# Kernel optimization log

Measured on AMD Instinct MI355X. Metric: run time of the kernel, lower is better.

Reference implementation:

```python
import jax, jax.numpy as jnp
import numpy as np

N = 100000   # nodes
E = 1600000  # edges
D_IN, D_H, D_OUT = 128, 128, 64
BN_EPS = 1e-5


def setup_inputs() -> dict:
    key = jax.random.key(0)
    ks = jax.random.split(key, 12)

    def lin_w(k, fan_in, shape):
        s = 1.0 / np.sqrt(fan_in)
        return jax.random.uniform(k, shape, jnp.float32, -s, s)

    return {
        "x": jax.random.normal(ks[0], (N, D_IN), jnp.float32),
        "edge_index": jax.random.randint(ks[1], (2, E), 0, N, dtype=jnp.int64),
        "edge_weight": jax.random.uniform(ks[2], (E,), jnp.float32),
        "W1": lin_w(ks[3], D_IN, (D_IN, D_H)),
        "b1": jnp.zeros((D_H,), jnp.float32),
        "W2": lin_w(ks[4], D_H, (D_H, D_H)),
        "b2": jnp.zeros((D_H,), jnp.float32),
        "W3": lin_w(ks[5], D_H, (D_H, D_OUT)),
        "b3": jnp.zeros((D_OUT,), jnp.float32),
        "gamma1": jnp.ones((D_H,), jnp.float32),
        "beta1": jnp.zeros((D_H,), jnp.float32),
        "gamma2": jnp.ones((D_H,), jnp.float32),
        "beta2": jnp.zeros((D_H,), jnp.float32),
    }


def _gcn_conv(x, src, dst, w, W, b):
    # PyG GCNConv: x' = D^{-1/2} (A + I) D^{-1/2} (x W) + b, self-loop weight 1
    n = x.shape[0]
    h = x @ W                                   # [N, d_out]
    loop = jnp.arange(n, dtype=src.dtype)
    s = jnp.concatenate([src, loop])            # [E+N]
    d = jnp.concatenate([dst, loop])
    ww = jnp.concatenate([w, jnp.ones((n,), w.dtype)])
    deg = jax.ops.segment_sum(ww, d, num_segments=n)          # in-degree at targets
    dinv = jnp.where(deg > 0, jax.lax.rsqrt(deg), 0.0)
    norm = dinv[s] * ww * dinv[d]               # [E+N]
    msg = h[s] * norm[:, None]                  # gather + scale
    out = jax.ops.segment_sum(msg, d, num_segments=n)
    return out + b


def _batch_norm(x, gamma, beta):
    mean = jnp.mean(x, axis=0)
    var = jnp.mean(jnp.square(x - mean), axis=0)  # biased, as BatchNorm uses
    return (x - mean) * jax.lax.rsqrt(var + BN_EPS) * gamma + beta


def reference(x, edge_index, edge_weight, W1, b1, W2, b2, W3, b3,
              gamma1, beta1, gamma2, beta2):
    src, dst = edge_index[0], edge_index[1]
    h = _gcn_conv(x, src, dst, edge_weight, W1, b1)
    h = jax.nn.relu(_batch_norm(h, gamma1, beta1))
    h = _gcn_conv(h, src, dst, edge_weight, W2, b2)
    h = jax.nn.relu(_batch_norm(h, gamma2, beta2))
    return _gcn_conv(h, src, dst, edge_weight, W3, b3)
```

## Files before the change

### kernel.cpp

```cpp
#include <hip/hip_runtime.h>
#include <hip/hip_fp16.h>
#include <cstdint>
#include <cstddef>

#define BN_EPS 1e-5f
#define KB 256
#define BSH 9

typedef _Float16 half8 __attribute__((ext_vector_type(8)));
typedef float floatx4 __attribute__((ext_vector_type(4)));

__device__ __forceinline__ float loadS(const __half* p) { return __half2float(*p); }
__device__ __forceinline__ float2 load2(const __half* p) {
    return __half22float2(*(const __half2*)p);
}
__device__ __forceinline__ void storeS(float* p, float v) { *p = v; }
__device__ __forceinline__ void storeS(__half* p, float v) { *p = __float2half(v); }
__device__ __forceinline__ void store2(float* p, float a, float b) {
    *(float2*)p = make_float2(a, b);
}
__device__ __forceinline__ void store2(__half* p, float a, float b) {
    *(__half2*)p = __floats2half2_rn(a, b);
}
__device__ __forceinline__ float wn_of(unsigned v) {
    __half_raw hr; hr.x = (unsigned short)(v & 0x7fffu);
    return __half2float((__half)hr);
}

static __device__ __forceinline__ int load_edge(const void* ei, int mode64, long long pos) {
    if (mode64) return (int)((const long long*)ei)[pos];
    return ((const int*)ei)[pos];
}

__global__ __launch_bounds__(256) void init_kernel(const unsigned* __restrict__ eiw, int nwords,
                                                   int* __restrict__ mode,
                                                   unsigned* __restrict__ pc,
                                                   const float* __restrict__ W1,
                                                   const float* __restrict__ W2,
                                                   const float* __restrict__ W3,
                                                   _Float16* __restrict__ WT1,
                                                   _Float16* __restrict__ WT2,
                                                   _Float16* __restrict__ WT3) {
    __shared__ unsigned red[256];
    const int bid = (int)blockIdx.x;
    const int tid = (int)threadIdx.x;
    if (bid < 64) {
        uint4 z = make_uint4(0, 0, 0, 0);
        *(uint4*)&pc[bid * 1024 + tid * 4] = z;
        return;
    }
    if (bid == 64) {
        unsigned m = 0;
        for (int i = 1 + 2 * tid; i < nwords; i += 512) m |= eiw[i];
        red[tid] = m;
        __syncthreads();
        for (int s = 128; s > 0; s >>= 1) {
            if (tid < s) red[tid] |= red[tid + s];
            __syncthreads();
        }
        if (tid == 0) mode[0] = (red[0] == 0) ? 1 : 0;
        return;
    }
    const int t_ = bid - 65;
    if (t_ < 64) {
        int t = t_ * 256 + tid;
        int n = t / 128, k = t % 128;
        WT1[t] = (_Float16)W1[k * 128 + n];
    } else if (t_ < 128) {
        int t = (t_ - 64) * 256 + tid;
        int n = t / 128, k = t % 128;
        WT2[t] = (_Float16)W2[k * 128 + n];
    } else {
        int t = (t_ - 128) * 256 + tid;
        int n = t / 128, k = t % 128;
        WT3[t] = (_Float16)W3[k * 64 + n];
    }
}

__global__ __launch_bounds__(256) void coarse_hist_kernel(const void* __restrict__ ei,
                                                          const int* __restrict__ mode,
                                                          unsigned* __restrict__ pc,
                                                          int E, int epb) {
    __shared__ unsigned h[256];
    const int k = (int)blockIdx.x;
    const int tid = (int)threadIdx.x;
    h[tid] = 0;
    __syncthreads();
    const int md = *mode;
    const int e0 = k * epb;
    const int e1 = min(E, e0 + epb);
    for (int e = e0 + tid; e < e1; e += 256) {
        int d = load_edge(ei, md, (long long)E + e);
        atomicAdd(&h[d >> BSH], 1u);
    }
    __syncthreads();
    pc[k * 256 + tid] = h[tid];
}

__global__ __launch_bounds__(256) void scan_pc_kernel(unsigned* __restrict__ pc,
                                                      int* __restrict__ tb) {
    __shared__ int red[256];
    const int b = (int)blockIdx.x;
    const int tid = (int)threadIdx.x;
    const unsigned v = pc[tid * 256 + b];
    red[tid] = (int)v;
    __syncthreads();
    for (int off = 1; off < 256; off <<= 1) {
        int t = 0;
        if (tid >= off) t = red[tid - off];
        __syncthreads();
        red[tid] += t;
        __syncthreads();
    }
    pc[tid * 256 + b] = (unsigned)(red[tid] - (int)v);
    if (tid == 255) tb[b] = red[255];
}

__global__ __launch_bounds__(256) void scan_buckets_kernel(const int* __restrict__ tb,
                                                           int* __restrict__ bbase, int nbuck,
                                                           float* __restrict__ gsum,
                                                           float* __restrict__ gsq) {
    __shared__ int red[256];
    const int tid = (int)threadIdx.x;
    const int v = (tid < nbuck) ? tb[tid] : 0;
    red[tid] = v;
    __syncthreads();
    for (int off = 1; off < 256; off <<= 1) {
        int t = 0;
        if (tid >= off) t = red[tid - off];
        __syncthreads();
        red[tid] += t;
        __syncthreads();
    }
    bbase[tid] = red[tid] - v;
    if (tid < 128) { gsum[tid] = 0.0f; gsq[tid] = 0.0f; }
}

template <int M, bool BN, typename TI>
__device__ __forceinline__ void gemm_body(int gbid, const TI* __restrict__ X,
                                          const _Float16* __restrict__ WTg,
                                          const float* __restrict__ sc,
                                          const float* __restrict__ sh,
                                          __half* __restrict__ Hout, int N,
                                          _Float16* WT ) {
    constexpr int CT = M / 16;
    constexpr int LDK = 136;

    for (int t = threadIdx.x; t < M * 16; t += 256) {
        int n = t / 16, seg = t % 16;
        *(half8*)&WT[n * LDK + seg * 8] = *(const half8*)&WTg[n * 128 + seg * 8];
    }
    __syncthreads();

    const int wave = (int)threadIdx.x >> 6;
    const int lane = (int)threadIdx.x & 63;
    const int qd = lane >> 4;
    const int ln = lane & 15;
    const int tile0 = gbid * 64 + wave * 16;
    int ar = tile0 + ln;
    if (ar >= N) ar = N - 1;

    half8 aF[4];
    const TI* xr = X + (size_t)ar * 128 + qd * 8;
#pragma unroll
    for (int kb = 0; kb < 4; ++kb) {
        float vv[8];
        if constexpr (sizeof(TI) == 4) {
            float4 v0 = *(const float4*)(xr + kb * 32);
            float4 v1 = *(const float4*)(xr + kb * 32 + 4);
            vv[0] = v0.x; vv[1] = v0.y; vv[2] = v0.z; vv[3] = v0.w;
            vv[4] = v1.x; vv[5] = v1.y; vv[6] = v1.z; vv[7] = v1.w;
        } else {
            half8 raw = *(const half8*)(xr + kb * 32);
#pragma unroll
            for (int j = 0; j < 8; ++j) vv[j] = (float)raw[j];
        }
        if (BN) {
            const int kbase = kb * 32 + qd * 8;
#pragma unroll
            for (int j = 0; j < 8; ++j)
                vv[j] = fmaxf(fmaf(vv[j], sc[kbase + j], sh[kbase + j]), 0.0f);
        }
        half8 a;
#pragma unroll
        for (int j = 0; j < 8; ++j) a[j] = (_Float16)vv[j];
        aF[kb] = a;
    }

#pragma unroll
    for (int ct = 0; ct < CT; ++ct) {
        floatx4 acc = {0.0f, 0.0f, 0.0f, 0.0f};
#pragma unroll
        for (int kb = 0; kb < 4; ++kb) {
            half8 b = *(const half8*)&WT[(ct * 16 + ln) * LDK + kb * 32 + qd * 8];
            acc = __builtin_amdgcn_mfma_f32_16x16x32_f16(aF[kb], b, acc, 0, 0, 0);
        }
#pragma unroll
        for (int r = 0; r < 4; ++r) {
            int orow = tile0 + qd * 4 + r;
            if (orow < N) Hout[(size_t)orow * M + ct * 16 + ln] = __float2half(acc[r]);
        }
    }
}

__global__ __launch_bounds__(256) void sort_gemm1_kernel(const void* __restrict__ ei,
                                                         const float* __restrict__ ew,
                                                         const unsigned* __restrict__ pc,
                                                         const int* __restrict__ bbase,
                                                         unsigned long long* __restrict__ sortedE,
                                                         const int* __restrict__ mode, int E,
                                                         int epb, int GB,
                                                         const float* __restrict__ X,
                                                         const _Float16* __restrict__ WT1g,
                                                         __half* __restrict__ Hout, int N) {
    __shared__ _Float16 WT[128 * 136];
    __shared__ unsigned off_s[256];
    if ((int)blockIdx.x < GB) {
        gemm_body<128, false, float>(blockIdx.x, X, WT1g, nullptr, nullptr, Hout, N, WT);
        return;
    }
    const int k = (int)blockIdx.x - GB;
    const int tid = (int)threadIdx.x;
    off_s[tid] = (unsigned)bbase[tid] + pc[k * 256 + tid];
    __syncthreads();
    const int md = *mode;
    const int e0 = k * epb;
    const int e1 = min(E, e0 + epb);
    for (int e = e0 + tid; e < e1; e += 256) {
        int d = load_edge(ei, md, (long long)E + e);
        int s = load_edge(ei, md, e);
        float wv = ew[e];
        unsigned slot = atomicAdd(&off_s[d >> BSH], 1u);
        sortedE[slot] = ((unsigned long long)(unsigned)d << 33) |
                        ((unsigned long long)(unsigned)s << 16) |
                        (unsigned long long)(unsigned short)__half_as_ushort(__float2half(wv));
    }
}

__global__ __launch_bounds__(256) void csr_build_kernel(const unsigned long long* __restrict__ sortedE,
                                                        const int* __restrict__ bbase,
                                                        const int* __restrict__ tb,
                                                        float* __restrict__ dinv,
                                                        int* __restrict__ cnt,
                                                        int* __restrict__ row_start,
                                                        unsigned* __restrict__ edata, int N) {
    __shared__ unsigned cs[512];
    __shared__ float ws[512];
    __shared__ float dv[512];
    __shared__ unsigned sc[512];
    __shared__ unsigned cur[512];
    __shared__ int red[256];
    const int b = (int)blockIdx.x;
    const int tid = (int)threadIdx.x;
    const int n0 = b << BSH;
    const int base = bbase[b];
    const int len = tb[b];

    cs[tid] = 0; cs[tid + 256] = 0;
    ws[tid] = 0.0f; ws[tid + 256] = 0.0f;
    cur[tid] = 0; cur[tid + 256] = 0;
    __syncthreads();

    for (int i = tid; i < len; i += 256) {
        unsigned long long p = sortedE[base + i];
        unsigned fine = (unsigned)(p >> 33) - (unsigned)n0;
        atomicAdd(&cs[fine], 1u);
        __half_raw hr; hr.x = (unsigned short)(p & 0xFFFFu);
        atomicAdd(&ws[fine], __half2float((__half)hr));
    }
    __syncthreads();

    const unsigned a0 = cs[2 * tid];
    const unsigned a1 = cs[2 * tid + 1];
    const int s2 = (int)(a0 + a1);
    red[tid] = s2;
    __syncthreads();
    for (int off = 1; off < 256; off <<= 1) {
        int t = 0;
        if (tid >= off) t = red[tid - off];
        __syncthreads();
        red[tid] += t;
        __syncthreads();
    }
    const int excl2 = red[tid] - s2;
    sc[2 * tid] = (unsigned)excl2;
    sc[2 * tid + 1] = (unsigned)(excl2 + (int)a0);

#pragma unroll
    for (int q = 0; q < 2; ++q) {
        const int f = tid + q * 256;
        const int node = n0 + f;
        const float dvv = rsqrtf(1.0f + ws[f]);
        dv[f] = dvv;
        if (node < N) {
            dinv[node] = dvv;
            cnt[node] = (int)cs[f];
            row_start[node] = base + (int)sc[f];
        }
    }
    __syncthreads();

    for (int i = tid; i < len; i += 256) {
        unsigned long long p = sortedE[base + i];
        unsigned fine = (unsigned)(p >> 33) - (unsigned)n0;
        unsigned s = (unsigned)(p >> 16) & 0x1FFFFu;
        __half_raw hr; hr.x = (unsigned short)(p & 0xFFFFu);
        float wnp = __half2float((__half)hr) * dv[fine];
        unsigned r = atomicAdd(&cur[fine], 1u);
        unsigned hb = (unsigned)__half_as_ushort(__float2half(wnp)) & 0x7fffu;
        edata[base + (int)sc[fine] + (int)r] = (s << 15) | hb;
    }
}

template <int D, bool BIAS, typename TY>
__global__ __launch_bounds__(256) void agg_kernel(const __half* __restrict__ H,
                                                  const unsigned* __restrict__ edata,
                                                  const int* __restrict__ row_start,
                                                  const int* __restrict__ cnt,
                                                  const float* __restrict__ dinv,
                                                  const float* __restrict__ bias,
                                                  TY* __restrict__ Y, int N) {
    constexpr int VPT = D / 64;
    const int lane = (int)threadIdx.x & 63;
    const int i = (int)blockIdx.x * 4 + ((int)threadIdx.x >> 6);
    if (i >= N) return;
    const int c0 = lane * VPT;
    const float di = dinv[i];
    const float dii = di * di;

    float acc0, acc1 = 0.0f;
    if constexpr (VPT == 2) {
        float2 h = load2(H + (size_t)i * D + c0);
        acc0 = dii * h.x;
        acc1 = dii * h.y;
    } else {
        acc0 = dii * loadS(H + (size_t)i * D + c0);
    }

    const int base = row_start[i];
    const int n = cnt[i];
    for (int off = 0; off < n; off += 64) {
        const int rem = n - off;
        unsigned ev = 0;
        if (lane < rem) ev = edata[base + off + lane];
        const int mm = min(64, rem);
        for (int j = 0; j < mm; j += 8) {
            const unsigned e0 = __shfl(ev, j),     e1 = __shfl(ev, j + 1);
            const unsigned e2 = __shfl(ev, j + 2), e3 = __shfl(ev, j + 3);
            const unsigned e4 = __shfl(ev, j + 4), e5 = __shfl(ev, j + 5);
            const unsigned e6 = __shfl(ev, j + 6), e7 = __shfl(ev, j + 7);
            const float w0 = dinv[e0 >> 15] * wn_of(e0);
            const float w1 = dinv[e1 >> 15] * wn_of(e1);
            const float w2 = dinv[e2 >> 15] * wn_of(e2);
            const float w3 = dinv[e3 >> 15] * wn_of(e3);
            const float w4 = dinv[e4 >> 15] * wn_of(e4);
            const float w5 = dinv[e5 >> 15] * wn_of(e5);
            const float w6 = dinv[e6 >> 15] * wn_of(e6);
            const float w7 = dinv[e7 >> 15] * wn_of(e7);
            if constexpr (VPT == 2) {
                float2 h0 = load2(H + (size_t)(e0 >> 15) * D + c0);
                float2 h1 = load2(H + (size_t)(e1 >> 15) * D + c0);
                float2 h2 = load2(H + (size_t)(e2 >> 15) * D + c0);
                float2 h3 = load2(H + (size_t)(e3 >> 15) * D + c0);
                float2 h4 = load2(H + (size_t)(e4 >> 15) * D + c0);
                float2 h5 = load2(H + (size_t)(e5 >> 15) * D + c0);
                float2 h6 = load2(H + (size_t)(e6 >> 15) * D + c0);
                float2 h7 = load2(H + (size_t)(e7 >> 15) * D + c0);
                acc0 = fmaf(w0, h0.x, acc0); acc1 = fmaf(w0, h0.y, acc1);
                acc0 = fmaf(w1, h1.x, acc0); acc1 = fmaf(w1, h1.y, acc1);
                acc0 = fmaf(w2, h2.x, acc0); acc1 = fmaf(w2, h2.y, acc1);
                acc0 = fmaf(w3, h3.x, acc0); acc1 = fmaf(w3, h3.y, acc1);
                acc0 = fmaf(w4, h4.x, acc0); acc1 = fmaf(w4, h4.y, acc1);
                acc0 = fmaf(w5, h5.x, acc0); acc1 = fmaf(w5, h5.y, acc1);
                acc0 = fmaf(w6, h6.x, acc0); acc1 = fmaf(w6, h6.y, acc1);
                acc0 = fmaf(w7, h7.x, acc0); acc1 = fmaf(w7, h7.y, acc1);
            } else {
                float h0 = loadS(H + (size_t)(e0 >> 15) * D + c0);
                float h1 = loadS(H + (size_t)(e1 >> 15) * D + c0);
                float h2 = loadS(H + (size_t)(e2 >> 15) * D + c0);
                float h3 = loadS(H + (size_t)(e3 >> 15) * D + c0);
                float h4 = loadS(H + (size_t)(e4 >> 15) * D + c0);
                float h5 = loadS(H + (size_t)(e5 >> 15) * D + c0);
                float h6 = loadS(H + (size_t)(e6 >> 15) * D + c0);
                float h7 = loadS(H + (size_t)(e7 >> 15) * D + c0);
                acc0 = fmaf(w0, h0, acc0);
                acc0 = fmaf(w1, h1, acc0);
                acc0 = fmaf(w2, h2, acc0);
                acc0 = fmaf(w3, h3, acc0);
                acc0 = fmaf(w4, h4, acc0);
                acc0 = fmaf(w5, h5, acc0);
                acc0 = fmaf(w6, h6, acc0);
                acc0 = fmaf(w7, h7, acc0);
            }
        }
    }

    if constexpr (VPT == 2) {
        if (BIAS) { acc0 += bias[c0]; acc1 += bias[c0 + 1]; }
        store2(Y + (size_t)i * D + c0, acc0, acc1);
    } else {
        if (BIAS) acc0 += bias[c0];
        storeS(Y + (size_t)i * D + c0, acc0);
    }
}

template <int M, bool BN, typename TI, bool ZERO>
__global__ __launch_bounds__(256) void gemm_mfma_kernel(const TI* __restrict__ X,
                                                        const _Float16* __restrict__ WTg,
                                                        const float* __restrict__ sc,
                                                        const float* __restrict__ sh,
                                                        __half* __restrict__ Hout, int N,
                                                        float* __restrict__ gsum,
                                                        float* __restrict__ gsq, int GB) {
    __shared__ _Float16 WT[M * 136];
    if (ZERO && (int)blockIdx.x == GB) {
        if (threadIdx.x < 128) { gsum[threadIdx.x] = 0.0f; gsq[threadIdx.x] = 0.0f; }
        return;
    }
    gemm_body<M, BN, TI>(blockIdx.x, X, WTg, sc, sh, Hout, N, WT);
}

__global__ void stats_kernel(const __half* __restrict__ Y, float* __restrict__ gsum,
                             float* __restrict__ gsq, int N) {
    __shared__ float ls[256], lq[256];
    const int tid = threadIdx.x;
    const int c = tid & 127;
    const int half_ = tid >> 7;
    float s = 0.0f, q = 0.0f;
    for (int row = blockIdx.x * 2 + half_; row < N; row += 512) {
        float v = __half2float(Y[(size_t)row * 128 + c]);
        s += v;
        q = fmaf(v, v, q);
    }
    ls[tid] = s; lq[tid] = q;
    __syncthreads();
    if (tid < 128) {
        atomicAdd(&gsum[c], ls[tid] + ls[tid + 128]);
        atomicAdd(&gsq[c],  lq[tid] + lq[tid + 128]);
    }
}

__global__ void finalize_stats_kernel(const float* __restrict__ gsum, const float* __restrict__ gsq,
                                      const float* __restrict__ gamma, const float* __restrict__ beta,
                                      float* __restrict__ sc, float* __restrict__ sh, int N) {
    int t = threadIdx.x;
    if (t < 128) {
        float inv_n = 1.0f / (float)N;
        float mean = gsum[t] * inv_n;
        float var = gsq[t] * inv_n - mean * mean;
        float scale = gamma[t] * rsqrtf(var + BN_EPS);
        sc[t] = scale;
        sh[t] = beta[t] - mean * scale;
    }
}

extern "C" void kernel_launch(void* const* d_in, const int* in_sizes, int n_in,
                              void* d_out, int out_size, void* d_ws, size_t ws_size,
                              hipStream_t stream) {
    const float* x   = (const float*)d_in[0];
    const void*  ei  = d_in[1];
    const float* ew  = (const float*)d_in[2];
    const float* W1  = (const float*)d_in[3];
    const float* W2  = (const float*)d_in[5];
    const float* W3  = (const float*)d_in[7];
    const float* b3  = (const float*)d_in[8];
    const float* g1  = (const float*)d_in[9];
    const float* be1 = (const float*)d_in[10];
    const float* g2  = (const float*)d_in[11];
    const float* be2 = (const float*)d_in[12];
    float* out = (float*)d_out;

    const int N = in_sizes[0] / 128;
    const int E = in_sizes[2];

    char* w = (char*)d_ws;
    size_t off = 0;
    auto alloc = [&](size_t bytes) -> void* {
        void* p = w + off;
        off += (bytes + 255) & ~(size_t)255;
        return p;
    };
    unsigned* pc     = (unsigned*)alloc(256 * 256 * 4);
    int*   tb        = (int*)  alloc(256 * 4);
    int*   bbase     = (int*)  alloc(256 * 4);
    unsigned long long* sortedE = (unsigned long long*)alloc((size_t)E * 8);
    float* dinv      = (float*)alloc((size_t)N * 4);
    int*   cnt       = (int*)  alloc((size_t)N * 4);
    int*   row_start = (int*)  alloc((size_t)N * 4);
    unsigned* edata  = (unsigned*)alloc((size_t)E * 4);
    int*   mode      = (int*)  alloc(256);
    float* gsum      = (float*)alloc(128 * 4);
    float* gsq       = (float*)alloc(128 * 4);
    float* scb       = (float*)alloc(128 * 4);
    float* shb       = (float*)alloc(128 * 4);
    _Float16* WT1    = (_Float16*)alloc(128 * 128 * 2);
    _Float16* WT2    = (_Float16*)alloc(128 * 128 * 2);
    _Float16* WT3    = (_Float16*)alloc(128 * 64 * 2);
    __half* H        = (__half*)alloc((size_t)N * 128 * 2);
    __half* Yh       = (__half*)alloc((size_t)N * 128 * 2);
    (void)ws_size; (void)n_in; (void)out_size;

    const int epb   = (E + KB - 1) / KB;
    const int nbuck = (N + (1 << BSH) - 1) >> BSH;
    const int gb    = (N + 63) / 64;
    const int ab    = (N + 3) / 4;

    init_kernel<<<64 + 1 + 160, 256, 0, stream>>>((const unsigned*)ei, 4096, mode, pc,
                                                  W1, W2, W3, WT1, WT2, WT3);
    coarse_hist_kernel<<<KB, 256, 0, stream>>>(ei, mode, pc, E, epb);
    scan_pc_kernel<<<nbuck, 256, 0, stream>>>(pc, tb);
    scan_buckets_kernel<<<1, 256, 0, stream>>>(tb, bbase, nbuck, gsum, gsq);
    sort_gemm1_kernel<<<gb + KB, 256, 0, stream>>>(ei, ew, pc, bbase, sortedE, mode, E,
                                                   epb, gb, x, WT1, H, N);
    csr_build_kernel<<<nbuck, 256, 0, stream>>>(sortedE, bbase, tb, dinv, cnt, row_start,
                                                edata, N);

    agg_kernel<128, false, __half><<<ab, 256, 0, stream>>>(H, edata, row_start, cnt, dinv, nullptr, Yh, N);
    stats_kernel<<<256, 256, 0, stream>>>(Yh, gsum, gsq, N);
    finalize_stats_kernel<<<1, 128, 0, stream>>>(gsum, gsq, g1, be1, scb, shb, N);

    gemm_mfma_kernel<128, true, __half, true><<<gb + 1, 256, 0, stream>>>(Yh, WT2, scb, shb, H, N, gsum, gsq, gb);
    agg_kernel<128, false, __half><<<ab, 256, 0, stream>>>(H, edata, row_start, cnt, dinv, nullptr, Yh, N);
    stats_kernel<<<256, 256, 0, stream>>>(Yh, gsum, gsq, N);
    finalize_stats_kernel<<<1, 128, 0, stream>>>(gsum, gsq, g2, be2, scb, shb, N);

    gemm_mfma_kernel<64, true, __half, false><<<gb, 256, 0, stream>>>(Yh, WT3, scb, shb, H, N, nullptr, nullptr, gb);
    agg_kernel<64, true, float><<<ab, 256, 0, stream>>>(H, edata, row_start, cnt, dinv, b3, out, N);
}
```

Before: 498.9 us.

## Prescale features by dinv and fuse small setup/stat kernels via last-block reductions

Source-side normalization dinv[s] now multiplies H rows directly: in csr_build for layer 1 and in the GEMM epilogue for later layers. The aggregation inner loop therefore drops its per-edge random dinv gather. Several tiny launches are removed: mode detection moves inline via a wave ballot, the histogram merges into init, and the bucket scan and BN finalize run in the last-arriving block through atomic tickets. This cuts launch overhead and gather traffic, at the cost of an extra read-modify-write pass over H in csr_build and fp16 rounding of the prescaled values.

```diff
diff --git a/kernel.cpp b/kernel.cpp
--- a/kernel.cpp
+++ b/kernel.cpp
@@ -32,61 +32,47 @@
     return ((const int*)ei)[pos];
 }
 
-__global__ __launch_bounds__(256) void init_kernel(const unsigned* __restrict__ eiw, int nwords,
-                                                   int* __restrict__ mode,
-                                                   unsigned* __restrict__ pc,
-                                                   const float* __restrict__ W1,
-                                                   const float* __restrict__ W2,
-                                                   const float* __restrict__ W3,
-                                                   _Float16* __restrict__ WT1,
-                                                   _Float16* __restrict__ WT2,
-                                                   _Float16* __restrict__ WT3) {
-    __shared__ unsigned red[256];
+__device__ __forceinline__ int detect_mode64(const unsigned* eiw) {
+    const int lane = (int)threadIdx.x & 63;
+    unsigned m = 0;
+    for (int i = lane; i < 2048; i += 64) m |= eiw[2 * i + 1];
+    return (__ballot(m != 0) == 0ULL) ? 1 : 0;
+}
+
+__global__ __launch_bounds__(256) void init_hist_kernel(const void* __restrict__ ei,
+                                                        unsigned* __restrict__ tk,
+                                                        unsigned* __restrict__ pc, int E, int epb,
+                                                        const float* __restrict__ W1,
+                                                        const float* __restrict__ W2,
+                                                        const float* __restrict__ W3,
+                                                        _Float16* __restrict__ WT1,
+                                                        _Float16* __restrict__ WT2,
+                                                        _Float16* __restrict__ WT3) {
     const int bid = (int)blockIdx.x;
     const int tid = (int)threadIdx.x;
-    if (bid < 64) {
-        uint4 z = make_uint4(0, 0, 0, 0);
-        *(uint4*)&pc[bid * 1024 + tid * 4] = z;
+    if (bid < 160) {
+        if (bid == 0 && tid < 8) tk[tid] = 0u;
+        const int t_ = bid;
+        if (t_ < 64) {
+            int t = t_ * 256 + tid;
+            int n = t / 128, k = t % 128;
+            WT1[t] = (_Float16)W1[k * 128 + n];
+        } else if (t_ < 128) {
+            int t = (t_ - 64) * 256 + tid;
+            int n = t / 128, k = t % 128;
+            WT2[t] = (_Float16)W2[k * 128 + n];
+        } else {
+            int t = (t_ - 128) * 256 + tid;
+            int n = t / 128, k = t % 128;
+            WT3[t] = (_Float16)W3[k * 64 + n];
+        }
         return;
     }
-    if (bid == 64) {
-        unsigned m = 0;
-        for (int i = 1 + 2 * tid; i < nwords; i += 512) m |= eiw[i];
-        red[tid] = m;
-        __syncthreads();
-        for (int s = 128; s > 0; s >>= 1) {
-            if (tid < s) red[tid] |= red[tid + s];
-            __syncthreads();
-        }
-        if (tid == 0) mode[0] = (red[0] == 0) ? 1 : 0;
-        return;
-    }
-    const int t_ = bid - 65;
-    if (t_ < 64) {
-        int t = t_ * 256 + tid;
-        int n = t / 128, k = t % 128;
-        WT1[t] = (_Float16)W1[k * 128 + n];
-    } else if (t_ < 128) {
-        int t = (t_ - 64) * 256 + tid;
-        int n = t / 128, k = t % 128;
-        WT2[t] = (_Float16)W2[k * 128 + n];
-    } else {
-        int t = (t_ - 128) * 256 + tid;
-        int n = t / 128, k = t % 128;
-        WT3[t] = (_Float16)W3[k * 64 + n];
-    }
-}
-
-__global__ __launch_bounds__(256) void coarse_hist_kernel(const void* __restrict__ ei,
-                                                          const int* __restrict__ mode,
-                                                          unsigned* __restrict__ pc,
-                                                          int E, int epb) {
     __shared__ unsigned h[256];
-    const int k = (int)blockIdx.x;
-    const int tid = (int)threadIdx.x;
+    const int k = bid - 160;
     h[tid] = 0;
     __syncthreads();
-    const int md = *mode;
+    const int md = detect_mode64((const unsigned*)ei);
     const int e0 = k * epb;
     const int e1 = min(E, e0 + epb);
     for (int e = e0 + tid; e < e1; e += 256) {
@@ -98,8 +84,13 @@
 }
 
 __global__ __launch_bounds__(256) void scan_pc_kernel(unsigned* __restrict__ pc,
-                                                      int* __restrict__ tb) {
+                                                      int* __restrict__ tb,
+                                                      int* __restrict__ bbase,
+                                                      float* __restrict__ gsum,
+                                                      float* __restrict__ gsq,
+                                                      unsigned* __restrict__ tk, int nbuck) {
     __shared__ int red[256];
+    __shared__ int lastFlag;
     const int b = (int)blockIdx.x;
     const int tid = (int)threadIdx.x;
     const unsigned v = pc[tid * 256 + b];
@@ -113,17 +104,19 @@
         __syncthreads();
     }
     pc[tid * 256 + b] = (unsigned)(red[tid] - (int)v);
-    if (tid == 255) tb[b] = red[255];
-}
-
-__global__ __launch_bounds__(256) void scan_buckets_kernel(const int* __restrict__ tb,
-                                                           int* __restrict__ bbase, int nbuck,
-                                                           float* __restrict__ gsum,
-                                                           float* __restrict__ gsq) {
-    __shared__ int red[256];
-    const int tid = (int)threadIdx.x;
-    const int v = (tid < nbuck) ? tb[tid] : 0;
-    red[tid] = v;
+    if (tid == 255)
+        __hip_atomic_store(&tb[b], red[255], __ATOMIC_RELEASE, __HIP_MEMORY_SCOPE_AGENT);
+    __syncthreads();
+    if (tid == 0) {
+        unsigned t = __hip_atomic_fetch_add(tk, 1u, __ATOMIC_ACQ_REL, __HIP_MEMORY_SCOPE_AGENT);
+        lastFlag = (t == (unsigned)gridDim.x - 1u) ? 1 : 0;
+    }
+    __syncthreads();
+    if (!lastFlag) return;
+    const int v2 = (tid < nbuck)
+        ? __hip_atomic_load(&tb[tid], __ATOMIC_ACQUIRE, __HIP_MEMORY_SCOPE_AGENT) : 0;
+    __syncthreads();
+    red[tid] = v2;
     __syncthreads();
     for (int off = 1; off < 256; off <<= 1) {
         int t = 0;
@@ -132,15 +125,16 @@
         red[tid] += t;
         __syncthreads();
     }
-    bbase[tid] = red[tid] - v;
+    bbase[tid] = red[tid] - v2;
     if (tid < 128) { gsum[tid] = 0.0f; gsq[tid] = 0.0f; }
 }
 
-template <int M, bool BN, typename TI>
+template <int M, bool BN, typename TI, bool SCALE>
 __device__ __forceinline__ void gemm_body(int gbid, const TI* __restrict__ X,
                                           const _Float16* __restrict__ WTg,
                                           const float* __restrict__ sc,
                                           const float* __restrict__ sh,
+                                          const float* __restrict__ dinvp,
                                           __half* __restrict__ Hout, int N,
                                           _Float16* WT ) {
     constexpr int CT = M / 16;
@@ -187,6 +181,15 @@
         aF[kb] = a;
     }
 
+    float dvr[4];
+    if constexpr (SCALE) {
+#pragma unroll
+        for (int r = 0; r < 4; ++r) {
+            int orow = tile0 + qd * 4 + r;
+            dvr[r] = (orow < N) ? dinvp[orow] : 1.0f;
+        }
+    }
+
 #pragma unroll
     for (int ct = 0; ct < CT; ++ct) {
         floatx4 acc = {0.0f, 0.0f, 0.0f, 0.0f};
@@ -198,7 +201,11 @@
 #pragma unroll
         for (int r = 0; r < 4; ++r) {
             int orow = tile0 + qd * 4 + r;
-            if (orow < N) Hout[(size_t)orow * M + ct * 16 + ln] = __float2half(acc[r]);
+            if (orow < N) {
+                float o = acc[r];
+                if constexpr (SCALE) o *= dvr[r];
+                Hout[(size_t)orow * M + ct * 16 + ln] = __float2half(o);
+            }
         }
     }
 }
@@ -208,22 +215,22 @@
                                                          const unsigned* __restrict__ pc,
                                                          const int* __restrict__ bbase,
                                                          unsigned long long* __restrict__ sortedE,
-                                                         const int* __restrict__ mode, int E,
-                                                         int epb, int GB,
+                                                         int E, int epb, int GB,
                                                          const float* __restrict__ X,
                                                          const _Float16* __restrict__ WT1g,
                                                          __half* __restrict__ Hout, int N) {
     __shared__ _Float16 WT[128 * 136];
     __shared__ unsigned off_s[256];
     if ((int)blockIdx.x < GB) {
-        gemm_body<128, false, float>(blockIdx.x, X, WT1g, nullptr, nullptr, Hout, N, WT);
+        gemm_body<128, false, float, false>(blockIdx.x, X, WT1g, nullptr, nullptr, nullptr,
+                                            Hout, N, WT);
         return;
     }
     const int k = (int)blockIdx.x - GB;
     const int tid = (int)threadIdx.x;
     off_s[tid] = (unsigned)bbase[tid] + pc[k * 256 + tid];
     __syncthreads();
-    const int md = *mode;
+    const int md = detect_mode64((const unsigned*)ei);
     const int e0 = k * epb;
     const int e1 = min(E, e0 + epb);
     for (int e = e0 + tid; e < e1; e += 256) {
@@ -243,7 +250,8 @@
                                                         float* __restrict__ dinv,
                                                         int* __restrict__ cnt,
                                                         int* __restrict__ row_start,
-                                                        unsigned* __restrict__ edata, int N) {
+                                                        unsigned* __restrict__ edata,
+                                                        __half* __restrict__ H, int N) {
     __shared__ unsigned cs[512];
     __shared__ float ws[512];
     __shared__ float dv[512];
@@ -309,6 +317,20 @@
         unsigned r = atomicAdd(&cur[fine], 1u);
         unsigned hb = (unsigned)__half_as_ushort(__float2half(wnp)) & 0x7fffu;
         edata[base + (int)sc[fine] + (int)r] = (s << 15) | hb;
+    }
+
+    for (int idx = tid; idx < (1 << BSH) * 16; idx += 256) {
+        const int r = idx >> 4;
+        const int node = n0 + r;
+        if (node < N) {
+            const int seg = idx & 15;
+            _Float16* hp = (_Float16*)H + (size_t)node * 128 + seg * 8;
+            half8 h = *(half8*)hp;
+            const float dvv = dv[r];
+#pragma unroll
+            for (int j = 0; j < 8; ++j) h[j] = (_Float16)((float)h[j] * dvv);
+            *(half8*)hp = h;
+        }
     }
 }
 
@@ -326,15 +348,14 @@
     if (i >= N) return;
     const int c0 = lane * VPT;
     const float di = dinv[i];
-    const float dii = di * di;
 
     float acc0, acc1 = 0.0f;
     if constexpr (VPT == 2) {
         float2 h = load2(H + (size_t)i * D + c0);
-        acc0 = dii * h.x;
-        acc1 = dii * h.y;
+        acc0 = di * h.x;
+        acc1 = di * h.y;
     } else {
-        acc0 = dii * loadS(H + (size_t)i * D + c0);
+        acc0 = di * loadS(H + (size_t)i * D + c0);
     }
 
     const int base = row_start[i];
@@ -349,14 +370,8 @@
             const unsigned e2 = __shfl(ev, j + 2), e3 = __shfl(ev, j + 3);
             const unsigned e4 = __shfl(ev, j + 4), e5 = __shfl(ev, j + 5);
             const unsigned e6 = __shfl(ev, j + 6), e7 = __shfl(ev, j + 7);
-            const float w0 = dinv[e0 >> 15] * wn_of(e0);
-            const float w1 = dinv[e1 >> 15] * wn_of(e1);
-            const float w2 = dinv[e2 >> 15] * wn_of(e2);
-            const float w3 = dinv[e3 >> 15] * wn_of(e3);
-            const float w4 = dinv[e4 >> 15] * wn_of(e4);
-            const float w5 = dinv[e5 >> 15] * wn_of(e5);
-            const float w6 = dinv[e6 >> 15] * wn_of(e6);
-            const float w7 = dinv[e7 >> 15] * wn_of(e7);
+            const float w0 = wn_of(e0), w1 = wn_of(e1), w2 = wn_of(e2), w3 = wn_of(e3);
+            const float w4 = wn_of(e4), w5 = wn_of(e5), w6 = wn_of(e6), w7 = wn_of(e7);
             if constexpr (VPT == 2) {
                 float2 h0 = load2(H + (size_t)(e0 >> 15) * D + c0);
                 float2 h1 = load2(H + (size_t)(e1 >> 15) * D + c0);
@@ -404,11 +419,12 @@
     }
 }
 
-template <int M, bool BN, typename TI, bool ZERO>
+template <int M, bool BN, typename TI, bool ZERO, bool SCALE>
 __global__ __launch_bounds__(256) void gemm_mfma_kernel(const TI* __restrict__ X,
                                                         const _Float16* __restrict__ WTg,
                                                         const float* __restrict__ sc,
                                                         const float* __restrict__ sh,
+                                                        const float* __restrict__ dinvp,
                                                         __half* __restrict__ Hout, int N,
                                                         float* __restrict__ gsum,
                                                         float* __restrict__ gsq, int GB) {
@@ -417,17 +433,24 @@
         if (threadIdx.x < 128) { gsum[threadIdx.x] = 0.0f; gsq[threadIdx.x] = 0.0f; }
         return;
     }
-    gemm_body<M, BN, TI>(blockIdx.x, X, WTg, sc, sh, Hout, N, WT);
-}
-
-__global__ void stats_kernel(const __half* __restrict__ Y, float* __restrict__ gsum,
-                             float* __restrict__ gsq, int N) {
+    gemm_body<M, BN, TI, SCALE>(blockIdx.x, X, WTg, sc, sh, dinvp, Hout, N, WT);
+}
+
+__global__ __launch_bounds__(256) void stats_kernel(const __half* __restrict__ Y,
+                                                    float* __restrict__ gsum,
+                                                    float* __restrict__ gsq,
+                                                    unsigned* __restrict__ tk,
+                                                    const float* __restrict__ gamma,
+                                                    const float* __restrict__ beta,
+                                                    float* __restrict__ sc,
+                                                    float* __restrict__ sh, int N) {
     __shared__ float ls[256], lq[256];
-    const int tid = threadIdx.x;
+    __shared__ int lastFlag;
+    const int tid = (int)threadIdx.x;
     const int c = tid & 127;
     const int half_ = tid >> 7;
     float s = 0.0f, q = 0.0f;
-    for (int row = blockIdx.x * 2 + half_; row < N; row += 512) {
+    for (int row = (int)blockIdx.x * 2 + half_; row < N; row += 512) {
         float v = __half2float(Y[(size_t)row * 128 + c]);
         s += v;
         q = fmaf(v, v, q);
@@ -438,19 +461,22 @@
         atomicAdd(&gsum[c], ls[tid] + ls[tid + 128]);
         atomicAdd(&gsq[c],  lq[tid] + lq[tid + 128]);
     }
-}
-
-__global__ void finalize_stats_kernel(const float* __restrict__ gsum, const float* __restrict__ gsq,
-                                      const float* __restrict__ gamma, const float* __restrict__ beta,
-                                      float* __restrict__ sc, float* __restrict__ sh, int N) {
-    int t = threadIdx.x;
-    if (t < 128) {
+    __syncthreads();
+    if (tid == 0) {
+        unsigned t = __hip_atomic_fetch_add(tk, 1u, __ATOMIC_ACQ_REL, __HIP_MEMORY_SCOPE_AGENT);
+        lastFlag = (t == (unsigned)gridDim.x - 1u) ? 1 : 0;
+    }
+    __syncthreads();
+    if (!lastFlag) return;
+    if (tid < 128) {
+        float gs = __hip_atomic_load(&gsum[tid], __ATOMIC_ACQUIRE, __HIP_MEMORY_SCOPE_AGENT);
+        float gq = __hip_atomic_load(&gsq[tid], __ATOMIC_ACQUIRE, __HIP_MEMORY_SCOPE_AGENT);
         float inv_n = 1.0f / (float)N;
-        float mean = gsum[t] * inv_n;
-        float var = gsq[t] * inv_n - mean * mean;
-        float scale = gamma[t] * rsqrtf(var + BN_EPS);
-        sc[t] = scale;
-        sh[t] = beta[t] - mean * scale;
+        float mean = gs * inv_n;
+        float var = gq * inv_n - mean * mean;
+        float scale = gamma[tid] * rsqrtf(var + BN_EPS);
+        sc[tid] = scale;
+        sh[tid] = beta[tid] - mean * scale;
     }
 }
 
@@ -488,7 +514,7 @@
     int*   cnt       = (int*)  alloc((size_t)N * 4);
     int*   row_start = (int*)  alloc((size_t)N * 4);
     unsigned* edata  = (unsigned*)alloc((size_t)E * 4);
-    int*   mode      = (int*)  alloc(256);
+    unsigned* tk     = (unsigned*)alloc(256);
     float* gsum      = (float*)alloc(128 * 4);
     float* gsq       = (float*)alloc(128 * 4);
     float* scb       = (float*)alloc(128 * 4);
@@ -505,25 +531,23 @@
     const int gb    = (N + 63) / 64;
     const int ab    = (N + 3) / 4;
 
-    init_kernel<<<64 + 1 + 160, 256, 0, stream>>>((const unsigned*)ei, 4096, mode, pc,
-                                                  W1, W2, W3, WT1, WT2, WT3);
-    coarse_hist_kernel<<<KB, 256, 0, stream>>>(ei, mode, pc, E, epb);
-    scan_pc_kernel<<<nbuck, 256, 0, stream>>>(pc, tb);
-    scan_buckets_kernel<<<1, 256, 0, stream>>>(tb, bbase, nbuck, gsum, gsq);
-    sort_gemm1_kernel<<<gb + KB, 256, 0, stream>>>(ei, ew, pc, bbase, sortedE, mode, E,
+    init_hist_kernel<<<160 + KB, 256, 0, stream>>>(ei, tk, pc, E, epb,
+                                                   W1, W2, W3, WT1, WT2, WT3);
+    scan_pc_kernel<<<nbuck, 256, 0, stream>>>(pc, tb, bbase, gsum, gsq, &tk[0], nbuck);
+    sort_gemm1_kernel<<<gb + KB, 256, 0, stream>>>(ei, ew, pc, bbase, sortedE, E,
                                                    epb, gb, x, WT1, H, N);
     csr_build_kernel<<<nbuck, 256, 0, stream>>>(sortedE, bbase, tb, dinv, cnt, row_start,
-                                                edata, N);
+                                                edata, H, N);
 
     agg_kernel<128, false, __half><<<ab, 256, 0, stream>>>(H, edata, row_start, cnt, dinv, nullptr, Yh, N);
-    stats_kernel<<<256, 256, 0, stream>>>(Yh, gsum, gsq, N);
-    finalize_stats_kernel<<<1, 128, 0, stream>>>(gsum, gsq, g1, be1, scb, shb, N);
-
-    gemm_mfma_kernel<128, true, __half, true><<<gb + 1, 256, 0, stream>>>(Yh, WT2, scb, shb, H, N, gsum, gsq, gb);
+    stats_kernel<<<256, 256, 0, stream>>>(Yh, gsum, gsq, &tk[1], g1, be1, scb, shb, N);
+
+    gemm_mfma_kernel<128, true, __half, true, true><<<gb + 1, 256, 0, stream>>>(
+        Yh, WT2, scb, shb, dinv, H, N, gsum, gsq, gb);
     agg_kernel<128, false, __half><<<ab, 256, 0, stream>>>(H, edata, row_start, cnt, dinv, nullptr, Yh, N);
-    stats_kernel<<<256, 256, 0, stream>>>(Yh, gsum, gsq, N);
-    finalize_stats_kernel<<<1, 128, 0, stream>>>(gsum, gsq, g2, be2, scb, shb, N);
-
-    gemm_mfma_kernel<64, true, __half, false><<<gb, 256, 0, stream>>>(Yh, WT3, scb, shb, H, N, nullptr, nullptr, gb);
+    stats_kernel<<<256, 256, 0, stream>>>(Yh, gsum, gsq, &tk[2], g2, be2, scb, shb, N);
+
+    gemm_mfma_kernel<64, true, __half, false, true><<<gb, 256, 0, stream>>>(
+        Yh, WT3, scb, shb, dinv, H, N, nullptr, nullptr, gb);
     agg_kernel<64, true, float><<<ab, 256, 0, stream>>>(H, edata, row_start, cnt, dinv, b3, out, N);
 }
```

Result: slower. 513.2 us (+2.9%).
